# Performance work log

Hardware: AMD Instinct MI355X
Metric: run time of the kernel (lower is better)

The kernel has to match this reference:

```python
import jax, jax.numpy as jnp
import numpy as np
import math

DIM = 1024

def setup_inputs() -> dict:
    key = jax.random.key(0)
    ks = jax.random.split(key, 5)
    X = jax.random.normal(ks[0], (4, 2048, DIM), dtype=jnp.float32)
    # Linear params (stored as [in, out] so y = x @ W + b)
    W_in = jax.random.normal(ks[1], (DIM, 3 * DIM), dtype=jnp.float32) / math.sqrt(DIM)
    b_in = jnp.zeros((3 * DIM,), dtype=jnp.float32)
    W_out = jax.random.normal(ks[2], (DIM, DIM), dtype=jnp.float32) / math.sqrt(DIM)
    b_out = jnp.zeros((DIM,), dtype=jnp.float32)
    return {"X": X, "W_in": W_in, "b_in": b_in, "W_out": W_out, "b_out": b_out}

def reference(X, W_in, b_in, W_out, b_out):
    dim = X.shape[-1]
    QKV = X @ W_in + b_in                       # [B, S, 3*dim]
    Q, K, V = jnp.split(QKV, 3, axis=-1)        # each [B, S, dim]
    scores = jnp.einsum('bqd,bkd->bqk', Q, K) / math.sqrt(dim)  # [B, S, S]
    attn = jax.nn.softmax(scores, axis=-1)
    out = jnp.einsum('bqk,bkd->bqd', attn, V)   # [B, S, dim]
    return out @ W_out + b_out
```

## Files before the change

kernel.cpp:

```cpp
#include <hip/hip_runtime.h>
#include <hip/hip_bf16.h>
#include <math.h>

typedef __attribute__((ext_vector_type(8))) __bf16 bf16x8;
typedef __attribute__((ext_vector_type(4))) float f32x4;

#define DIM 1024
#define SEQ 2048
#define BATCH 4
#define ROWS (BATCH*SEQ)

__device__ __forceinline__ unsigned short f2bf(float f) {
  unsigned int u = __float_as_uint(f);
  u += 0x7FFF + ((u >> 16) & 1);
  return (unsigned short)(u >> 16);
}

__device__ __forceinline__ void gload_lds16(const void* g, void* lds) {
  __builtin_amdgcn_global_load_lds((__attribute__((address_space(1))) void*)g,
                                   (__attribute__((address_space(3))) void*)lds,
                                   16, 0, 0);
}

__global__ __launch_bounds__(256)
void conv_f32_bf16(const float* __restrict__ src, unsigned short* __restrict__ dst, int n8) {
  int i = blockIdx.x * blockDim.x + threadIdx.x;
  if (i >= n8) return;
  const float4* s = reinterpret_cast<const float4*>(src) + (size_t)i * 2;
  float4 a = s[0], b = s[1];
  union { unsigned short h[8]; uint4 v; } p;
  p.h[0]=f2bf(a.x); p.h[1]=f2bf(a.y); p.h[2]=f2bf(a.z); p.h[3]=f2bf(a.w);
  p.h[4]=f2bf(b.x); p.h[5]=f2bf(b.y); p.h[6]=f2bf(b.z); p.h[7]=f2bf(b.w);
  reinterpret_cast<uint4*>(dst)[i] = p.v;
}

__global__ __launch_bounds__(1024)
void transpose_weights(const float* __restrict__ W_in, unsigned short* __restrict__ WinT,
                       const float* __restrict__ W_out, unsigned short* __restrict__ WoutT) {
  __shared__ unsigned short tile[32][33];
  const int z = blockIdx.z;
  const float* src; unsigned short* dst; int ldsrc, bx;
  if (z < 3) { src = W_in;  dst = WinT;  ldsrc = 3 * DIM; bx = z * 32 + blockIdx.x; }
  else       { src = W_out; dst = WoutT; ldsrc = DIM;     bx = blockIdx.x; }
  int tx = threadIdx.x, ty = threadIdx.y;
  int r = blockIdx.y * 32 + ty, c = bx * 32 + tx;
  tile[ty][tx] = f2bf(src[(size_t)r * ldsrc + c]);
  __syncthreads();
  dst[(size_t)(bx * 32 + ty) * DIM + blockIdx.y * 32 + tx] = tile[tx][ty];
}

#define EPI_QKV 0
#define EPI_F32 1
#define EPI_BF16 2
#define EPI_BIAS_F32 3

template<int EPI>
__global__ __launch_bounds__(256, 3)
void gemm97(const unsigned short* __restrict__ A, int lda, size_t sA,
            const unsigned short* __restrict__ B, int ldb, size_t sB,
            void* __restrict__ C, int ldc, size_t sC,
            const float* __restrict__ bias, int K,
            unsigned short* __restrict__ VtOut, size_t sVt) {
  __shared__ unsigned short As[128 * 64];
  __shared__ unsigned short Bs[128 * 64];

  const int tid = threadIdx.x;
  const int lane = tid & 63, wave = tid >> 6;
  const int wr = wave >> 1, wc = wave & 1;
  const int fr = lane & 15, fk = lane >> 4;
  const int tileM = (EPI == EPI_QKV ? blockIdx.x : blockIdx.y) * 128;
  const int tileN = (EPI == EPI_QKV ? blockIdx.y : blockIdx.x) * 128;
  const unsigned short* Ab = A + (size_t)blockIdx.z * sA;
  const unsigned short* Bb = B + (size_t)blockIdx.z * sB;

  const int srow = tid >> 3;
  const int sg = (tid & 7) ^ (srow & 7);
  const int sp = (tid & 7) * 8;

  f32x4 acc[4][4];
#pragma unroll
  for (int m = 0; m < 4; ++m)
#pragma unroll
    for (int n = 0; n < 4; ++n) acc[m][n] = (f32x4){0.f, 0.f, 0.f, 0.f};

  for (int kt = 0; kt < K; kt += 64) {
    __syncthreads();
#pragma unroll
    for (int q = 0; q < 4; ++q) {
      int rl = q * 32 + srow;
      gload_lds16(Ab + (size_t)(tileM + rl) * lda + kt + sg * 8, &As[rl * 64 + sp]);
    }
#pragma unroll
    for (int q = 0; q < 4; ++q) {
      int rl = q * 32 + srow;
      gload_lds16(Bb + (size_t)(tileN + rl) * ldb + kt + sg * 8, &Bs[rl * 64 + sp]);
    }
    __syncthreads();

    bf16x8 af[4][2], bg[4][2];
#pragma unroll
    for (int m = 0; m < 4; ++m) {
      int row = wr * 64 + m * 16 + fr;
#pragma unroll
      for (int kk = 0; kk < 2; ++kk)
        af[m][kk] = *reinterpret_cast<const bf16x8*>(
            &As[row * 64 + (((kk * 4 + fk) ^ (row & 7)) << 3)]);
    }
#pragma unroll
    for (int n = 0; n < 4; ++n) {
      int row = wc * 64 + n * 16 + fr;
#pragma unroll
      for (int kk = 0; kk < 2; ++kk)
        bg[n][kk] = *reinterpret_cast<const bf16x8*>(
            &Bs[row * 64 + (((kk * 4 + fk) ^ (row & 7)) << 3)]);
    }
#pragma unroll
    for (int kk = 0; kk < 2; ++kk)
#pragma unroll
      for (int m = 0; m < 4; ++m)
#pragma unroll
        for (int n = 0; n < 4; ++n)
          acc[m][n] = __builtin_amdgcn_mfma_f32_16x16x32_bf16(af[m][kk], bg[n][kk], acc[m][n], 0, 0, 0);
  }

  if (EPI == EPI_QKV && tileN >= 2 * DIM) {
    const int b = tileM >> 11;
    const int sb0 = (tileM & (SEQ - 1)) + wr * 64;
    unsigned short* Vb = VtOut + (size_t)b * sVt;
#pragma unroll
    for (int m = 0; m < 4; ++m)
#pragma unroll
      for (int n = 0; n < 4; ++n) {
        int col = tileN + wc * 64 + n * 16 + fr;
        int d = col - 2 * DIM;
        int s = sb0 + m * 16 + fk * 4;
        union { unsigned short h[4]; uint2 u; } p;
#pragma unroll
        for (int j = 0; j < 4; ++j) p.h[j] = f2bf(acc[m][n][j] + bias[col]);
        *reinterpret_cast<uint2*>(&Vb[(size_t)d * SEQ + s]) = p.u;
      }
  } else {
#pragma unroll
    for (int m = 0; m < 4; ++m)
#pragma unroll
      for (int n = 0; n < 4; ++n)
#pragma unroll
        for (int j = 0; j < 4; ++j) {
          int row = tileM + wr * 64 + m * 16 + fk * 4 + j;
          int col = tileN + wc * 64 + n * 16 + fr;
          float v = acc[m][n][j];
          if (EPI == EPI_QKV) {
            v += bias[col];
            if (col < DIM) v *= 0.03125f;
            ((unsigned short*)C + (size_t)blockIdx.z * sC)[(size_t)row * ldc + col] = f2bf(v);
          } else if (EPI == EPI_BF16) {
            ((unsigned short*)C + (size_t)blockIdx.z * sC)[(size_t)row * ldc + col] = f2bf(v);
          } else if (EPI == EPI_BIAS_F32) {
            ((float*)C + (size_t)blockIdx.z * sC)[(size_t)row * ldc + col] = v + bias[col];
          } else {
            ((float*)C + (size_t)blockIdx.z * sC)[(size_t)row * ldc + col] = v;
          }
        }
  }
}

__global__ __launch_bounds__(256)
void softmax_kernel(float* __restrict__ S, size_t zstride) {
  __shared__ float red[8];
  float* row = S + (size_t)blockIdx.y * zstride + (size_t)blockIdx.x * SEQ;
  const int tid = threadIdx.x;
  const int lane = tid & 63, wave = tid >> 6;
  const float4* src = reinterpret_cast<const float4*>(row) + tid * 2;
  float4 a = src[0], b = src[1];
  float v[8] = {a.x, a.y, a.z, a.w, b.x, b.y, b.z, b.w};
  float m = v[0];
#pragma unroll
  for (int i = 1; i < 8; ++i) m = fmaxf(m, v[i]);
  for (int o = 32; o; o >>= 1) m = fmaxf(m, __shfl_xor(m, o));
  if (lane == 0) red[wave] = m;
  __syncthreads();
  m = fmaxf(fmaxf(red[0], red[1]), fmaxf(red[2], red[3]));
  float e[8], s = 0.f;
#pragma unroll
  for (int i = 0; i < 8; ++i) { e[i] = __expf(v[i] - m); s += e[i]; }
  for (int o = 32; o; o >>= 1) s += __shfl_xor(s, o);
  if (lane == 0) red[4 + wave] = s;
  __syncthreads();
  s = red[4] + red[5] + red[6] + red[7];
  float inv = 1.f / s;
  union { unsigned short h[8]; uint4 u; } p;
#pragma unroll
  for (int i = 0; i < 8; ++i) p.h[i] = f2bf(e[i] * inv);
  reinterpret_cast<uint4*>(row)[tid] = p.u;
}

extern "C" void kernel_launch(void* const* d_in, const int* in_sizes, int n_in,
                              void* d_out, int out_size, void* d_ws, size_t ws_size,
                              hipStream_t stream) {
  const float* X     = (const float*)d_in[0];
  const float* W_in  = (const float*)d_in[1];
  const float* b_in  = (const float*)d_in[2];
  const float* W_out = (const float*)d_in[3];
  const float* b_out = (const float*)d_in[4];
  float* out = (float*)d_out;
  char* ws = (char*)d_ws;

  size_t o = 0;
  auto alloc = [&](size_t bytes) { size_t r = o; o += (bytes + 255) & ~(size_t)255; return r; };
  unsigned short* Xbf   = (unsigned short*)(ws + alloc((size_t)ROWS * DIM * 2));
  unsigned short* WinT  = (unsigned short*)(ws + alloc((size_t)3 * DIM * DIM * 2));
  unsigned short* WoutT = (unsigned short*)(ws + alloc((size_t)DIM * DIM * 2));
  unsigned short* QKV   = (unsigned short*)(ws + alloc((size_t)ROWS * 3 * DIM * 2));
  unsigned short* Vt    = (unsigned short*)(ws + alloc((size_t)BATCH * DIM * SEQ * 2));
  size_t fixed = o;
  size_t per_batch = (((size_t)SEQ * SEQ * 4 + 255) & ~(size_t)255);
  int G = (ws_size >= fixed + 4 * per_batch) ? BATCH : 1;
  float* Sc = (float*)(ws + alloc((size_t)G * SEQ * SEQ * 4));
  unsigned short* Ob = Xbf;

  conv_f32_bf16<<<(ROWS * DIM / 8 + 255) / 256, 256, 0, stream>>>(X, Xbf, ROWS * DIM / 8);
  transpose_weights<<<dim3(32, 32, 4), dim3(32, 32), 0, stream>>>(W_in, WinT, W_out, WoutT);
  gemm97<EPI_QKV><<<dim3(ROWS / 128, 3 * DIM / 128, 1), 256, 0, stream>>>(
      Xbf, DIM, 0, WinT, DIM, 0, QKV, 3 * DIM, 0, b_in, DIM,
      Vt, (size_t)DIM * SEQ);

  for (int b0 = 0; b0 < BATCH; b0 += G) {
    const unsigned short* Qb = QKV + (size_t)b0 * SEQ * 3 * DIM;
    const unsigned short* Kb = Qb + DIM;
    gemm97<EPI_F32><<<dim3(SEQ / 128, SEQ / 128, G), 256, 0, stream>>>(
        Qb, 3 * DIM, (size_t)SEQ * 3 * DIM, Kb, 3 * DIM, (size_t)SEQ * 3 * DIM,
        Sc, SEQ, (size_t)SEQ * SEQ, nullptr, DIM, nullptr, 0);
    softmax_kernel<<<dim3(SEQ, G), 256, 0, stream>>>(Sc, (size_t)SEQ * SEQ);
    gemm97<EPI_BF16><<<dim3(DIM / 128, SEQ / 128, G), 256, 0, stream>>>(
        (const unsigned short*)Sc, 2 * SEQ, (size_t)2 * SEQ * SEQ,
        Vt + (size_t)b0 * DIM * SEQ, SEQ, (size_t)DIM * SEQ,
        Ob + (size_t)b0 * SEQ * DIM, DIM, (size_t)SEQ * DIM, nullptr, SEQ, nullptr, 0);
  }
  gemm97<EPI_BIAS_F32><<<dim3(DIM / 128, ROWS / 128, 1), 256, 0, stream>>>(
      Ob, DIM, 0, WoutT, DIM, 0, out, DIM, 0, b_out, DIM, nullptr, 0);
}
```

Measured before the change: 204.0 us.

## Fuse softmax into score GEMM epilogue and PV GEMM prologue via row stats

Removes the standalone softmax pass. The QK^T GEMM epilogue now writes per-tile row max and sum-of-exp partials, a small kernel combines them into per-row max and inverse sum, and the PV GEMM reads the fp32 scores and applies exp and normalisation while staging A into LDS. This drops one full read and write of the SxS score matrix. The cost is that the PV GEMM now reads fp32 scores through registers instead of async bf16 global-to-LDS loads, and recomputes exp for each N-tile.

Measured after the change: 237.4 us. +16.4%, slower.

```diff
diff --git a/kernel.cpp b/kernel.cpp
--- a/kernel.cpp
+++ b/kernel.cpp
@@ -9,6 +9,7 @@
 #define SEQ 2048
 #define BATCH 4
 #define ROWS (BATCH*SEQ)
+#define NBX 16
 
 __device__ __forceinline__ unsigned short f2bf(float f) {
   unsigned int u = __float_as_uint(f);
@@ -49,9 +50,26 @@
   dst[(size_t)(bx * 32 + ty) * DIM + blockIdx.y * 32 + tx] = tile[tx][ty];
 }
 
+__global__ __launch_bounds__(256)
+void stat_combine(const float2* __restrict__ pstat, float2* __restrict__ rowstat) {
+  const int r = blockIdx.x * 256 + threadIdx.x;
+  const int z = blockIdx.y;
+  float2 v[NBX];
+  float M = -3.4e38f;
+#pragma unroll
+  for (int i = 0; i < NBX; ++i) {
+    v[i] = pstat[((size_t)z * NBX + i) * SEQ + r];
+    M = fmaxf(M, v[i].x);
+  }
+  float S = 0.f;
+#pragma unroll
+  for (int i = 0; i < NBX; ++i) S += v[i].y * __expf(v[i].x - M);
+  rowstat[(size_t)z * SEQ + r] = make_float2(M, 1.f / S);
+}
+
 #define EPI_QKV 0
-#define EPI_F32 1
-#define EPI_BF16 2
+#define EPI_SC  1
+#define EPI_PVF 2
 #define EPI_BIAS_F32 3
 
 template<int EPI>
@@ -60,7 +78,8 @@
             const unsigned short* __restrict__ B, int ldb, size_t sB,
             void* __restrict__ C, int ldc, size_t sC,
             const float* __restrict__ bias, int K,
-            unsigned short* __restrict__ VtOut, size_t sVt) {
+            unsigned short* __restrict__ VtOut, size_t sVt,
+            float2* __restrict__ pstat, const float2* __restrict__ rowstat) {
   __shared__ unsigned short As[128 * 64];
   __shared__ unsigned short Bs[128 * 64];
 
@@ -77,6 +96,15 @@
   const int sg = (tid & 7) ^ (srow & 7);
   const int sp = (tid & 7) * 8;
 
+  float mR[4], iR[4];
+  if constexpr (EPI == EPI_PVF) {
+#pragma unroll
+    for (int q = 0; q < 4; ++q) {
+      float2 st = rowstat[(size_t)blockIdx.z * SEQ + tileM + q * 32 + srow];
+      mR[q] = st.x; iR[q] = st.y;
+    }
+  }
+
   f32x4 acc[4][4];
 #pragma unroll
   for (int m = 0; m < 4; ++m)
@@ -85,15 +113,36 @@
 
   for (int kt = 0; kt < K; kt += 64) {
     __syncthreads();
-#pragma unroll
-    for (int q = 0; q < 4; ++q) {
-      int rl = q * 32 + srow;
-      gload_lds16(Ab + (size_t)(tileM + rl) * lda + kt + sg * 8, &As[rl * 64 + sp]);
-    }
 #pragma unroll
     for (int q = 0; q < 4; ++q) {
       int rl = q * 32 + srow;
       gload_lds16(Bb + (size_t)(tileN + rl) * ldb + kt + sg * 8, &Bs[rl * 64 + sp]);
+    }
+    if constexpr (EPI == EPI_PVF) {
+      const float* Af = (const float*)Ab;
+#pragma unroll
+      for (int q = 0; q < 4; ++q) {
+        int rl = q * 32 + srow;
+        const float* ap = Af + (size_t)(tileM + rl) * lda + kt + (tid & 7) * 8;
+        float4 x0 = *(const float4*)ap;
+        float4 x1 = *(const float4*)(ap + 4);
+        union { unsigned short h[8]; uint4 u; } pk;
+        pk.h[0] = f2bf(__expf(x0.x - mR[q]) * iR[q]);
+        pk.h[1] = f2bf(__expf(x0.y - mR[q]) * iR[q]);
+        pk.h[2] = f2bf(__expf(x0.z - mR[q]) * iR[q]);
+        pk.h[3] = f2bf(__expf(x0.w - mR[q]) * iR[q]);
+        pk.h[4] = f2bf(__expf(x1.x - mR[q]) * iR[q]);
+        pk.h[5] = f2bf(__expf(x1.y - mR[q]) * iR[q]);
+        pk.h[6] = f2bf(__expf(x1.z - mR[q]) * iR[q]);
+        pk.h[7] = f2bf(__expf(x1.w - mR[q]) * iR[q]);
+        *(uint4*)&As[rl * 64 + (((tid & 7) ^ (rl & 7)) << 3)] = pk.u;
+      }
+    } else {
+#pragma unroll
+      for (int q = 0; q < 4; ++q) {
+        int rl = q * 32 + srow;
+        gload_lds16(Ab + (size_t)(tileM + rl) * lda + kt + sg * 8, &As[rl * 64 + sp]);
+      }
     }
     __syncthreads();
 
@@ -153,7 +202,7 @@
             v += bias[col];
             if (col < DIM) v *= 0.03125f;
             ((unsigned short*)C + (size_t)blockIdx.z * sC)[(size_t)row * ldc + col] = f2bf(v);
-          } else if (EPI == EPI_BF16) {
+          } else if (EPI == EPI_PVF) {
             ((unsigned short*)C + (size_t)blockIdx.z * sC)[(size_t)row * ldc + col] = f2bf(v);
           } else if (EPI == EPI_BIAS_F32) {
             ((float*)C + (size_t)blockIdx.z * sC)[(size_t)row * ldc + col] = v + bias[col];
@@ -162,36 +211,41 @@
           }
         }
   }
-}
-
-__global__ __launch_bounds__(256)
-void softmax_kernel(float* __restrict__ S, size_t zstride) {
-  __shared__ float red[8];
-  float* row = S + (size_t)blockIdx.y * zstride + (size_t)blockIdx.x * SEQ;
-  const int tid = threadIdx.x;
-  const int lane = tid & 63, wave = tid >> 6;
-  const float4* src = reinterpret_cast<const float4*>(row) + tid * 2;
-  float4 a = src[0], b = src[1];
-  float v[8] = {a.x, a.y, a.z, a.w, b.x, b.y, b.z, b.w};
-  float m = v[0];
-#pragma unroll
-  for (int i = 1; i < 8; ++i) m = fmaxf(m, v[i]);
-  for (int o = 32; o; o >>= 1) m = fmaxf(m, __shfl_xor(m, o));
-  if (lane == 0) red[wave] = m;
-  __syncthreads();
-  m = fmaxf(fmaxf(red[0], red[1]), fmaxf(red[2], red[3]));
-  float e[8], s = 0.f;
-#pragma unroll
-  for (int i = 0; i < 8; ++i) { e[i] = __expf(v[i] - m); s += e[i]; }
-  for (int o = 32; o; o >>= 1) s += __shfl_xor(s, o);
-  if (lane == 0) red[4 + wave] = s;
-  __syncthreads();
-  s = red[4] + red[5] + red[6] + red[7];
-  float inv = 1.f / s;
-  union { unsigned short h[8]; uint4 u; } p;
-#pragma unroll
-  for (int i = 0; i < 8; ++i) p.h[i] = f2bf(e[i] * inv);
-  reinterpret_cast<uint4*>(row)[tid] = p.u;
+
+  if constexpr (EPI == EPI_SC) {
+    float* sm = (float*)As;
+    float* ss = sm + 256;
+    __syncthreads();
+#pragma unroll
+    for (int m = 0; m < 4; ++m)
+#pragma unroll
+      for (int j = 0; j < 4; ++j) {
+        float mx = fmaxf(fmaxf(acc[m][0][j], acc[m][1][j]), fmaxf(acc[m][2][j], acc[m][3][j]));
+        mx = fmaxf(mx, __shfl_xor(mx, 1));
+        mx = fmaxf(mx, __shfl_xor(mx, 2));
+        mx = fmaxf(mx, __shfl_xor(mx, 4));
+        mx = fmaxf(mx, __shfl_xor(mx, 8));
+        float se = __expf(acc[m][0][j] - mx) + __expf(acc[m][1][j] - mx) +
+                   __expf(acc[m][2][j] - mx) + __expf(acc[m][3][j] - mx);
+        se += __shfl_xor(se, 1);
+        se += __shfl_xor(se, 2);
+        se += __shfl_xor(se, 4);
+        se += __shfl_xor(se, 8);
+        if (fr == 0) {
+          int r = wr * 64 + m * 16 + fk * 4 + j;
+          sm[wc * 128 + r] = mx;
+          ss[wc * 128 + r] = se;
+        }
+      }
+    __syncthreads();
+    if (tid < 128) {
+      float m0 = sm[tid], m1 = sm[128 + tid];
+      float s0 = ss[tid], s1 = ss[128 + tid];
+      float M = fmaxf(m0, m1);
+      float S = s0 * __expf(m0 - M) + s1 * __expf(m1 - M);
+      pstat[((size_t)blockIdx.z * NBX + blockIdx.x) * SEQ + tileM + tid] = make_float2(M, S);
+    }
+  }
 }
 
 extern "C" void kernel_launch(void* const* d_in, const int* in_sizes, int n_in,
@@ -212,6 +266,8 @@
   unsigned short* WoutT = (unsigned short*)(ws + alloc((size_t)DIM * DIM * 2));
   unsigned short* QKV   = (unsigned short*)(ws + alloc((size_t)ROWS * 3 * DIM * 2));
   unsigned short* Vt    = (unsigned short*)(ws + alloc((size_t)BATCH * DIM * SEQ * 2));
+  float2*         Pst   = (float2*)(ws + alloc((size_t)BATCH * NBX * SEQ * 8));
+  float2*         Rst   = (float2*)(ws + alloc((size_t)BATCH * SEQ * 8));
   size_t fixed = o;
   size_t per_batch = (((size_t)SEQ * SEQ * 4 + 255) & ~(size_t)255);
   int G = (ws_size >= fixed + 4 * per_batch) ? BATCH : 1;
@@ -222,20 +278,23 @@
   transpose_weights<<<dim3(32, 32, 4), dim3(32, 32), 0, stream>>>(W_in, WinT, W_out, WoutT);
   gemm97<EPI_QKV><<<dim3(ROWS / 128, 3 * DIM / 128, 1), 256, 0, stream>>>(
       Xbf, DIM, 0, WinT, DIM, 0, QKV, 3 * DIM, 0, b_in, DIM,
-      Vt, (size_t)DIM * SEQ);
+      Vt, (size_t)DIM * SEQ, nullptr, nullptr);
 
   for (int b0 = 0; b0 < BATCH; b0 += G) {
     const unsigned short* Qb = QKV + (size_t)b0 * SEQ * 3 * DIM;
     const unsigned short* Kb = Qb + DIM;
-    gemm97<EPI_F32><<<dim3(SEQ / 128, SEQ / 128, G), 256, 0, stream>>>(
+    gemm97<EPI_SC><<<dim3(SEQ / 128, SEQ / 128, G), 256, 0, stream>>>(
         Qb, 3 * DIM, (size_t)SEQ * 3 * DIM, Kb, 3 * DIM, (size_t)SEQ * 3 * DIM,
-        Sc, SEQ, (size_t)SEQ * SEQ, nullptr, DIM, nullptr, 0);
-    softmax_kernel<<<dim3(SEQ, G), 256, 0, stream>>>(Sc, (size_t)SEQ * SEQ);
-    gemm97<EPI_BF16><<<dim3(DIM / 128, SEQ / 128, G), 256, 0, stream>>>(
-        (const unsigned short*)Sc, 2 * SEQ, (size_t)2 * SEQ * SEQ,
+        Sc, SEQ, (size_t)SEQ * SEQ, nullptr, DIM, nullptr, 0,
+        Pst + (size_t)b0 * NBX * SEQ, nullptr);
+    stat_combine<<<dim3(SEQ / 256, G), 256, 0, stream>>>(
+        Pst + (size_t)b0 * NBX * SEQ, Rst + (size_t)b0 * SEQ);
+    gemm97<EPI_PVF><<<dim3(DIM / 128, SEQ / 128, G), 256, 0, stream>>>(
+        (const unsigned short*)Sc, SEQ, (size_t)2 * SEQ * SEQ,
         Vt + (size_t)b0 * DIM * SEQ, SEQ, (size_t)DIM * SEQ,
-        Ob + (size_t)b0 * SEQ * DIM, DIM, (size_t)SEQ * DIM, nullptr, SEQ, nullptr, 0);
+        Ob + (size_t)b0 * SEQ * DIM, DIM, (size_t)SEQ * DIM, nullptr, SEQ,
+        nullptr, 0, nullptr, Rst + (size_t)b0 * SEQ);
   }
   gemm97<EPI_BIAS_F32><<<dim3(DIM / 128, ROWS / 128, 1), 256, 0, stream>>>(
-      Ob, DIM, 0, WoutT, DIM, 0, out, DIM, 0, b_out, DIM, nullptr, 0);
-}
+      Ob, DIM, 0, WoutT, DIM, 0, out, DIM, 0, b_out, DIM, nullptr, 0, nullptr, nullptr);
+}
```
